# Performance work log

Hardware: AMD Instinct MI355X
Metric: run time of the kernel (lower is better)

Reference implementation:

```python
import jax, jax.numpy as jnp
import numpy as np

N_EMBD = 128
N_HEADS = 8
HEAD_SIZE = N_EMBD // N_HEADS  # 16
EPS = 1e-5


def _layernorm(x, g, b):
    m = jnp.mean(x, axis=-1, keepdims=True)
    v = jnp.mean(jnp.square(x - m), axis=-1, keepdims=True)
    return (x - m) * jax.lax.rsqrt(v + EPS) * g + b


def setup_inputs() -> dict:
    key = jax.random.key(0)
    ks = jax.random.split(key, 12)
    B, T, D, H, HS = 16, 1024, N_EMBD, N_HEADS, HEAD_SIZE
    s = 1.0 / np.sqrt(D)
    inp = {
        "x": jax.random.normal(ks[0], (B, T, D), jnp.float32),
        # per-head QKV projections (stacked over heads; matches ModuleList of Linear(D, HS))
        "Wq": jax.random.uniform(ks[1], (H, D, HS), jnp.float32, -s, s),
        "bq": jnp.zeros((H, HS), jnp.float32),
        "Wk": jax.random.uniform(ks[2], (H, D, HS), jnp.float32, -s, s),
        "bk": jnp.zeros((H, HS), jnp.float32),
        "Wv": jax.random.uniform(ks[3], (H, D, HS), jnp.float32, -s, s),
        "bv": jnp.zeros((H, HS), jnp.float32),
        "Wp": jax.random.uniform(ks[4], (H * HS, D), jnp.float32, -s, s),
        "bp": jnp.zeros((D,), jnp.float32),
        "W1": jax.random.uniform(ks[5], (D, 4 * D), jnp.float32, -s, s),
        "b1": jnp.zeros((4 * D,), jnp.float32),
        "W2": jax.random.uniform(ks[6], (4 * D, D), jnp.float32, -1.0 / np.sqrt(4 * D), 1.0 / np.sqrt(4 * D)),
        "b2": jnp.zeros((D,), jnp.float32),
        "g1": jnp.ones((D,), jnp.float32),
        "be1": jnp.zeros((D,), jnp.float32),
        "g2": jnp.ones((D,), jnp.float32),
        "be2": jnp.zeros((D,), jnp.float32),
    }
    return inp


def reference(x, Wq, bq, Wk, bk, Wv, bv, Wp, bp, W1, b1, W2, b2, g1, be1, g2, be2):
    B, T, D = x.shape
    # batched per-head projections: [B,T,D] x [H,D,HS] -> [B,H,T,HS]
    q = jnp.einsum("btd,hds->bhts", x, Wq) + bq[None, :, None, :]
    k = jnp.einsum("btd,hds->bhts", x, Wk) + bk[None, :, None, :]
    v = jnp.einsum("btd,hds->bhts", x, Wv) + bv[None, :, None, :]
    scores = jnp.einsum("bhts,bhus->bhtu", q, k) / np.sqrt(HEAD_SIZE).astype(np.float32)
    tril = jnp.tril(jnp.ones((T, T), x.dtype))
    # faithful to source: multiplicative + additive mask (not -inf where)
    scores = scores * tril - 1e12 * (1.0 - tril)
    attn = jax.nn.softmax(scores, axis=-1)
    out = jnp.einsum("bhtu,bhus->bhts", attn, v)  # [B,H,T,HS]
    # concat heads in head order -> [B,T,H*HS]
    out = out.transpose(0, 2, 1, 3).reshape(B, T, -1)
    attn_out = out @ Wp + bp
    x = _layernorm(attn_out + x, g1, be1)
    h = jax.nn.gelu(x @ W1 + b1, approximate=False) @ W2 + b2
    x = _layernorm(h + x, g2, be2)
    return x
```

## Files before the change

kernel.cpp:

```cpp
#include <hip/hip_runtime.h>
#include <hip/hip_bf16.h>
#include <math.h>

constexpr int NB  = 16;
constexpr int NT  = 1024;
constexpr int ND  = 128;
constexpr int NH  = 8;
constexpr int NHS = 16;
constexpr int NDH = 512;
constexpr long NBT = (long)NB * NT;

typedef __attribute__((ext_vector_type(8))) short short8;
typedef __attribute__((ext_vector_type(4))) float f32x4;
typedef __attribute__((ext_vector_type(4))) unsigned short us4;

__device__ __forceinline__ unsigned short f2bf(float f) {
    __hip_bfloat16 h = __float2bfloat16(f);
    return *(unsigned short*)&h;
}

__device__ __forceinline__ short8 cvt8(const float* p) {
    const float4 f0 = *(const float4*)p;
    const float4 f1 = *(const float4*)(p + 4);
    union { short8 s; __hip_bfloat162 h[4]; } u;
    u.h[0] = __float22bfloat162_rn(make_float2(f0.x, f0.y));
    u.h[1] = __float22bfloat162_rn(make_float2(f0.z, f0.w));
    u.h[2] = __float22bfloat162_rn(make_float2(f1.x, f1.y));
    u.h[3] = __float22bfloat162_rn(make_float2(f1.z, f1.w));
    return u.s;
}

__device__ __forceinline__ float fast_gelu(float y) {
    const float t = y * y;
    const float u = __builtin_fmaf(y * 0.044715f, t, y);
    const float e = __builtin_amdgcn_exp2f(u * -2.302118131f);
    return y * __builtin_amdgcn_rcpf(1.0f + e);
}

__global__ __launch_bounds__(256) void k_prep(
    const float* __restrict__ Wq, const float* __restrict__ Wk,
    const float* __restrict__ Wv, __hip_bfloat16* __restrict__ Wqkvt)
{
    const int blk = blockIdx.x, tid = threadIdx.x;
    const int i0 = blk * 1024 + tid * 4;
    const int n = i0 >> 7, d0 = i0 & 127;
    const int sec = n >> 7, m = n & 127;
    const float* W = (sec == 0) ? Wq : (sec == 1) ? Wk : Wv;
    const float* src = W + (m >> 4) * 2048 + (m & 15);
    us4 v;
    #pragma unroll
    for (int j = 0; j < 4; ++j) v[j] = f2bf(src[(d0 + j) * 16]);
    *(us4*)((unsigned short*)Wqkvt + i0) = v;
}

__global__ __launch_bounds__(256) void k_qkv(
    const float* __restrict__ x, const __hip_bfloat16* __restrict__ Wqkvt,
    const float* __restrict__ bq, const float* __restrict__ bk,
    const float* __restrict__ bv,
    const float* __restrict__ Wp, const float* __restrict__ W1,
    const float* __restrict__ W2,
    __hip_bfloat16* __restrict__ Wpt, __hip_bfloat16* __restrict__ W1t,
    __hip_bfloat16* __restrict__ W2t,
    __hip_bfloat16* __restrict__ qo, __hip_bfloat16* __restrict__ ko,
    __hip_bfloat16* __restrict__ vo)
{
    __shared__ __align__(16) unsigned short st[32 * 392];
    const int tid = threadIdx.x;

    if (blockIdx.x >= 512) {
        const int blk = blockIdx.x - 512 + 48;
        us4 v;
        if (blk < 64) {
            const int i0 = (blk - 48) * 1024 + tid * 4;
            const int n = i0 >> 7, d0 = i0 & 127;
            #pragma unroll
            for (int j = 0; j < 4; ++j) v[j] = f2bf(Wp[(d0 + j) * 128 + n]);
            *(us4*)((unsigned short*)Wpt + i0) = v;
        } else if (blk < 128) {
            const int i0 = (blk - 64) * 1024 + tid * 4;
            const int n = i0 >> 7, d0 = i0 & 127;
            #pragma unroll
            for (int j = 0; j < 4; ++j) v[j] = f2bf(W1[(d0 + j) * 512 + n]);
            *(us4*)((unsigned short*)W1t + i0) = v;
        } else {
            const int i0 = (blk - 128) * 1024 + tid * 4;
            const int n = i0 >> 9, k0 = i0 & 511;
            #pragma unroll
            for (int j = 0; j < 4; ++j) v[j] = f2bf(W2[(k0 + j) * 128 + n]);
            *(us4*)((unsigned short*)W2t + i0) = v;
        }
        return;
    }

    const int w    = tid >> 6;
    const int lane = tid & 63;
    const int sL   = lane & 15;
    const int quad = lane >> 4;
    const int tok0 = blockIdx.x * 32;

    const unsigned short* W = (const unsigned short*)Wqkvt;

    short8 bx[2][4];
    #pragma unroll
    for (int tt = 0; tt < 2; ++tt)
        #pragma unroll
        for (int ks = 0; ks < 4; ++ks)
            bx[tt][ks] = cvt8(x + (size_t)(tok0 + tt * 16 + sL) * 128 + ks * 32 + quad * 8);

    f32x4 acc[6][2];
    #pragma unroll
    for (int ci = 0; ci < 6; ++ci)
        #pragma unroll
        for (int tt = 0; tt < 2; ++tt)
            acc[ci][tt] = (f32x4){0.f, 0.f, 0.f, 0.f};

    #pragma unroll
    for (int ks = 0; ks < 4; ++ks) {
        short8 aW[6];
        #pragma unroll
        for (int ci = 0; ci < 6; ++ci) {
            const int ct = w * 6 + ci;
            aW[ci] = *(const short8*)(W + (size_t)(ct * 16 + sL) * 128 + ks * 32 + quad * 8);
        }
        #pragma unroll
        for (int ci = 0; ci < 6; ++ci)
            #pragma unroll
            for (int tt = 0; tt < 2; ++tt)
                acc[ci][tt] = __builtin_amdgcn_mfma_f32_16x16x32_bf16(aW[ci], bx[tt][ks], acc[ci][tt], 0, 0, 0);
    }

    const float qscale = 0.3606737602f;
    #pragma unroll
    for (int ci = 0; ci < 6; ++ci) {
        const int ct = w * 6 + ci;
        const int kind = ct >> 3;
        const int ncc = (ct & 7) * 16 + quad * 4;
        const float4 bb = *(const float4*)(((kind == 0) ? bq : (kind == 1) ? bk : bv) + ncc);
        #pragma unroll
        for (int tt = 0; tt < 2; ++tt) {
            us4 v;
            #pragma unroll
            for (int r = 0; r < 4; ++r) {
                float val = acc[ci][tt][r] + ((const float*)&bb)[r];
                if (kind == 0) val *= qscale;
                v[r] = f2bf(val);
            }
            *(us4*)(st + (tt * 16 + sL) * 392 + ct * 16 + quad * 4) = v;
        }
    }
    __syncthreads();

    const int b = tok0 >> 10, tt0 = tok0 & 1023;
    {
        const int h = tid >> 5, tok = tid & 31;
        const unsigned short* sq = st + tok * 392 + h * 16;
        const unsigned short* sk = st + tok * 392 + 128 + h * 16;
        unsigned short* dq = (unsigned short*)qo + ((size_t)(b * 8 + h) * 1024 + tt0 + tok) * 16;
        unsigned short* dk = (unsigned short*)ko + ((size_t)(b * 8 + h) * 1024 + tt0 + tok) * 16;
        *(short8*)dq       = *(const short8*)sq;
        *(short8*)(dq + 8) = *(const short8*)(sq + 8);
        *(short8*)dk       = *(const short8*)sk;
        *(short8*)(dk + 8) = *(const short8*)(sk + 8);
    }
    if (tid < 128) {
        const int h = tid >> 4, s = tid & 15;
        unsigned short tmp[32];
        #pragma unroll
        for (int tok = 0; tok < 32; ++tok)
            tmp[tok] = st[tok * 392 + 256 + h * 16 + s];
        unsigned short* dv = (unsigned short*)vo + ((size_t)(b * 8 + h) * 16 + s) * 1024 + tt0;
        #pragma unroll
        for (int j = 0; j < 4; ++j)
            *(short8*)(dv + j * 8) = *(const short8*)(tmp + j * 8);
    }
}

__global__ __launch_bounds__(256) void k_attn(
    const __hip_bfloat16* __restrict__ qb, const __hip_bfloat16* __restrict__ kb,
    const __hip_bfloat16* __restrict__ vtb, __hip_bfloat16* __restrict__ att)
{
    const int bh   = blockIdx.x & 127;
    const int sub  = blockIdx.x >> 7;
    const int wave = threadIdx.x >> 6;
    const int lane = threadIdx.x & 63;
    const int sL   = lane & 15;
    const int q    = lane >> 4;
    const int b = bh >> 3, h = bh & 7;
    const int tile = sub * 4 + wave;

    const char* qbase = (const char*)qb  + (size_t)bh * NT * NHS * 2;
    const char* kbase = (const char*)kb  + (size_t)bh * NT * NHS * 2;
    const char* vbase = (const char*)vtb + (size_t)bh * NHS * NT * 2;

    const short8 zz = {0,0,0,0,0,0,0,0};

    const int t0 = tile * 16;
    const int tmy = t0 + sL;

    short8 bQ = zz;
    if (q < 2) bQ = *(const short8*)(qbase + (size_t)tmy * 32 + q * 16);

    f32x4 o = {0.f, 0.f, 0.f, 0.f};
    float lp = 0.f;

    const int nch = (t0 + 47) >> 5;
    for (int c = 0; c < nch; ++c) {
        const int u0 = c * 32;
        short8 aK0 = zz, aK1 = zz;
        if (q < 2) {
            aK0 = *(const short8*)(kbase + (size_t)(u0 + sL) * 32 + q * 16);
            aK1 = *(const short8*)(kbase + (size_t)(u0 + 16 + sL) * 32 + q * 16);
        }
        const f32x4 zc = {0.f, 0.f, 0.f, 0.f};
        f32x4 sT0 = __builtin_amdgcn_mfma_f32_16x16x32_bf16(aK0, bQ, zc, 0, 0, 0);
        f32x4 sT1 = __builtin_amdgcn_mfma_f32_16x16x32_bf16(aK1, bQ, zc, 0, 0, 0);

        int pk[4];
        if (u0 + 31 <= t0) {
            #pragma unroll
            for (int r = 0; r < 4; ++r) {
                const float p0 = __builtin_amdgcn_exp2f(sT0[r]);
                const float p1 = __builtin_amdgcn_exp2f(sT1[r]);
                lp += p0 + p1;
                __hip_bfloat162 hh = __float22bfloat162_rn(make_float2(p0, p1));
                pk[r] = *(int*)&hh;
            }
        } else {
            #pragma unroll
            for (int r = 0; r < 4; ++r) {
                const int ua = u0 + 4 * q + r;
                const float e0 = __builtin_amdgcn_exp2f(sT0[r]);
                const float e1 = __builtin_amdgcn_exp2f(sT1[r]);
                const float p0 = (ua      <= tmy) ? e0 : 0.f;
                const float p1 = (ua + 16 <= tmy) ? e1 : 0.f;
                lp += p0 + p1;
                __hip_bfloat162 hh = __float22bfloat162_rn(make_float2(p0, p1));
                pk[r] = *(int*)&hh;
            }
        }

        short8 bP;
        #pragma unroll
        for (int j = 0; j < 8; ++j) {
            const int srcq = ((q & 1) << 1) + (j >> 2);
            const int src  = (srcq << 4) + sL;
            const int g = __shfl(pk[j & 3], src);
            bP[j] = (short)((q < 2) ? (g & 0xffff) : ((unsigned)g >> 16));
        }

        const short8 aV = *(const short8*)(vbase + ((size_t)sL * NT + u0 + q * 8) * 2);
        o = __builtin_amdgcn_mfma_f32_16x16x32_bf16(aV, bP, o, 0, 0, 0);
    }

    float l = lp;
    l += __shfl_xor(l, 16);
    l += __shfl_xor(l, 32);
    const float inv = 1.0f / l;
    us4 res;
    res[0] = f2bf(o[0] * inv); res[1] = f2bf(o[1] * inv);
    res[2] = f2bf(o[2] * inv); res[3] = f2bf(o[3] * inv);
    *(us4*)((unsigned short*)att + ((size_t)b * NT + tmy) * ND + h * NHS + q * 4) = res;
}

__global__ __launch_bounds__(256) void k_tail(
    const __hip_bfloat16* __restrict__ attb, const __hip_bfloat16* __restrict__ Wpt,
    const __hip_bfloat16* __restrict__ W1t, const __hip_bfloat16* __restrict__ W2t,
    const float* __restrict__ x, const float* __restrict__ bp,
    const float* __restrict__ g1, const float* __restrict__ be1,
    const float* __restrict__ b1, const float* __restrict__ b2,
    const float* __restrict__ g2, const float* __restrict__ be2,
    float* __restrict__ out)
{
    __shared__ float ys[32][132];
    __shared__ __align__(16) unsigned short l1b[32 * 136];
    __shared__ __align__(16) unsigned short midb[32 * 528];
    const int w    = threadIdx.x >> 6;
    const int lane = threadIdx.x & 63;
    const int sL   = lane & 15;
    const int quad = lane >> 4;
    const int tok0 = blockIdx.x * 32;

    {
        const unsigned short* A = (const unsigned short*)attb;
        const unsigned short* W = (const unsigned short*)Wpt;
        short8 bfr[2][4];
        #pragma unroll
        for (int tt = 0; tt < 2; ++tt)
            #pragma unroll
            for (int ks = 0; ks < 4; ++ks)
                bfr[tt][ks] = *(const short8*)(A + (size_t)(tok0 + tt * 16 + sL) * 128 + ks * 32 + quad * 8);

        f32x4 acc[2][2];
        #pragma unroll
        for (int ci = 0; ci < 2; ++ci)
            #pragma unroll
            for (int tt = 0; tt < 2; ++tt)
                acc[ci][tt] = (f32x4){0.f, 0.f, 0.f, 0.f};

        #pragma unroll
        for (int ks = 0; ks < 4; ++ks) {
            short8 aW[2];
            #pragma unroll
            for (int ci = 0; ci < 2; ++ci)
                aW[ci] = *(const short8*)(W + (size_t)((w * 2 + ci) * 16 + sL) * 128 + ks * 32 + quad * 8);
            #pragma unroll
            for (int ci = 0; ci < 2; ++ci)
                #pragma unroll
                for (int tt = 0; tt < 2; ++tt)
                    acc[ci][tt] = __builtin_amdgcn_mfma_f32_16x16x32_bf16(aW[ci], bfr[tt][ks], acc[ci][tt], 0, 0, 0);
        }
        #pragma unroll
        for (int ci = 0; ci < 2; ++ci) {
            const int n0 = (w * 2 + ci) * 16 + quad * 4;
            const float4 bb = *(const float4*)(bp + n0);
            #pragma unroll
            for (int tt = 0; tt < 2; ++tt) {
                float4 v;
                v.x = acc[ci][tt][0] + bb.x; v.y = acc[ci][tt][1] + bb.y;
                v.z = acc[ci][tt][2] + bb.z; v.w = acc[ci][tt][3] + bb.w;
                *(float4*)(&ys[tt * 16 + sL][n0]) = v;
            }
        }
    }
    __syncthreads();

    const int tok = threadIdx.x >> 3;
    const int l8  = threadIdx.x & 7;
    const int c0  = l8 * 16;
    {
        float vals[16];
        float s = 0.f, s2 = 0.f;
        #pragma unroll
        for (int ch = 0; ch < 4; ++ch) {
            const float4 ly = *(const float4*)&ys[tok][c0 + ch * 4];
            const float4 gx = *(const float4*)(x + (size_t)(tok0 + tok) * 128 + c0 + ch * 4);
            vals[ch*4+0] = ly.x + gx.x; vals[ch*4+1] = ly.y + gx.y;
            vals[ch*4+2] = ly.z + gx.z; vals[ch*4+3] = ly.w + gx.w;
            #pragma unroll
            for (int j = 0; j < 4; ++j) { s += vals[ch*4+j]; s2 += vals[ch*4+j] * vals[ch*4+j]; }
        }
        #pragma unroll
        for (int off = 1; off <= 4; off <<= 1) {
            s  += __shfl_xor(s, off, 8);
            s2 += __shfl_xor(s2, off, 8);
        }
        const float mean = s * (1.0f / 128.0f);
        const float var  = s2 * (1.0f / 128.0f) - mean * mean;
        const float rstd = rsqrtf(var + 1e-5f);
        #pragma unroll
        for (int ch = 0; ch < 4; ++ch) {
            const float4 gg = *(const float4*)(g1 + c0 + ch * 4);
            const float4 bb = *(const float4*)(be1 + c0 + ch * 4);
            float ln0 = (vals[ch*4+0] - mean) * rstd * gg.x + bb.x;
            float ln1v = (vals[ch*4+1] - mean) * rstd * gg.y + bb.y;
            float ln2v = (vals[ch*4+2] - mean) * rstd * gg.z + bb.z;
            float ln3 = (vals[ch*4+3] - mean) * rstd * gg.w + bb.w;
            ys[tok][c0 + ch*4 + 0] = ln0;
            ys[tok][c0 + ch*4 + 1] = ln1v;
            ys[tok][c0 + ch*4 + 2] = ln2v;
            ys[tok][c0 + ch*4 + 3] = ln3;
            us4 lb;
            lb[0] = f2bf(ln0); lb[1] = f2bf(ln1v); lb[2] = f2bf(ln2v); lb[3] = f2bf(ln3);
            *(us4*)(l1b + tok * 136 + c0 + ch * 4) = lb;
        }
    }
    __syncthreads();

    {
        const unsigned short* W = (const unsigned short*)W1t;
        short8 bl[2][4];
        #pragma unroll
        for (int tt = 0; tt < 2; ++tt)
            #pragma unroll
            for (int ks = 0; ks < 4; ++ks)
                bl[tt][ks] = *(const short8*)(l1b + (tt * 16 + sL) * 136 + ks * 32 + quad * 8);

        f32x4 acc[8][2];
        #pragma unroll
        for (int ci = 0; ci < 8; ++ci)
            #pragma unroll
            for (int tt = 0; tt < 2; ++tt)
                acc[ci][tt] = (f32x4){0.f, 0.f, 0.f, 0.f};

        #pragma unroll
        for (int ks = 0; ks < 4; ++ks) {
            short8 aW[8];
            #pragma unroll
            for (int ci = 0; ci < 8; ++ci)
                aW[ci] = *(const short8*)(W + (size_t)((w * 8 + ci) * 16 + sL) * 128 + ks * 32 + quad * 8);
            #pragma unroll
            for (int ci = 0; ci < 8; ++ci)
                #pragma unroll
                for (int tt = 0; tt < 2; ++tt)
                    acc[ci][tt] = __builtin_amdgcn_mfma_f32_16x16x32_bf16(aW[ci], bl[tt][ks], acc[ci][tt], 0, 0, 0);
        }
        #pragma unroll
        for (int ci = 0; ci < 8; ++ci) {
            const int n0 = (w * 8 + ci) * 16 + quad * 4;
            const float4 bb = *(const float4*)(b1 + n0);
            #pragma unroll
            for (int tt = 0; tt < 2; ++tt) {
                us4 v;
                v[0] = f2bf(fast_gelu(acc[ci][tt][0] + bb.x));
                v[1] = f2bf(fast_gelu(acc[ci][tt][1] + bb.y));
                v[2] = f2bf(fast_gelu(acc[ci][tt][2] + bb.z));
                v[3] = f2bf(fast_gelu(acc[ci][tt][3] + bb.w));
                *(us4*)(midb + (tt * 16 + sL) * 528 + n0) = v;
            }
        }
    }
    __syncthreads();

    f32x4 acc2[2][2];
    #pragma unroll
    for (int ci = 0; ci < 2; ++ci)
        #pragma unroll
        for (int tt = 0; tt < 2; ++tt)
            acc2[ci][tt] = (f32x4){0.f, 0.f, 0.f, 0.f};
    {
        const unsigned short* W = (const unsigned short*)W2t;
        #pragma unroll
        for (int ks = 0; ks < 16; ++ks) {
            short8 bm0 = *(const short8*)(midb + (size_t)sL * 528 + ks * 32 + quad * 8);
            short8 bm1 = *(const short8*)(midb + (size_t)(16 + sL) * 528 + ks * 32 + quad * 8);
            short8 aW0 = *(const short8*)(W + (size_t)((w * 2) * 16 + sL) * 512 + ks * 32 + quad * 8);
            short8 aW1 = *(const short8*)(W + (size_t)((w * 2 + 1) * 16 + sL) * 512 + ks * 32 + quad * 8);
            acc2[0][0] = __builtin_amdgcn_mfma_f32_16x16x32_bf16(aW0, bm0, acc2[0][0], 0, 0, 0);
            acc2[0][1] = __builtin_amdgcn_mfma_f32_16x16x32_bf16(aW0, bm1, acc2[0][1], 0, 0, 0);
            acc2[1][0] = __builtin_amdgcn_mfma_f32_16x16x32_bf16(aW1, bm0, acc2[1][0], 0, 0, 0);
            acc2[1][1] = __builtin_amdgcn_mfma_f32_16x16x32_bf16(aW1, bm1, acc2[1][1], 0, 0, 0);
        }
    }
    __syncthreads();
    float* ys2 = (float*)midb;
    #pragma unroll
    for (int ci = 0; ci < 2; ++ci) {
        const int n0 = (w * 2 + ci) * 16 + quad * 4;
        const float4 bb = *(const float4*)(b2 + n0);
        #pragma unroll
        for (int tt = 0; tt < 2; ++tt) {
            float4 v;
            v.x = acc2[ci][tt][0] + bb.x; v.y = acc2[ci][tt][1] + bb.y;
            v.z = acc2[ci][tt][2] + bb.z; v.w = acc2[ci][tt][3] + bb.w;
            *(float4*)(ys2 + (tt * 16 + sL) * 132 + n0) = v;
        }
    }
    __syncthreads();

    {
        float vals[16];
        float s = 0.f, s2 = 0.f;
        #pragma unroll
        for (int ch = 0; ch < 4; ++ch) {
            const float4 ly = *(const float4*)(ys2 + tok * 132 + c0 + ch * 4);
            const float4 gx = *(const float4*)&ys[tok][c0 + ch * 4];
            vals[ch*4+0] = ly.x + gx.x; vals[ch*4+1] = ly.y + gx.y;
            vals[ch*4+2] = ly.z + gx.z; vals[ch*4+3] = ly.w + gx.w;
            #pragma unroll
            for (int j = 0; j < 4; ++j) { s += vals[ch*4+j]; s2 += vals[ch*4+j] * vals[ch*4+j]; }
        }
        #pragma unroll
        for (int off = 1; off <= 4; off <<= 1) {
            s  += __shfl_xor(s, off, 8);
            s2 += __shfl_xor(s2, off, 8);
        }
        const float mean = s * (1.0f / 128.0f);
        const float var  = s2 * (1.0f / 128.0f) - mean * mean;
        const float rstd = rsqrtf(var + 1e-5f);
        #pragma unroll
        for (int ch = 0; ch < 4; ++ch) {
            const float4 gg = *(const float4*)(g2 + c0 + ch * 4);
            const float4 bb = *(const float4*)(be2 + c0 + ch * 4);
            float4 ln;
            ln.x = (vals[ch*4+0] - mean) * rstd * gg.x + bb.x;
            ln.y = (vals[ch*4+1] - mean) * rstd * gg.y + bb.y;
            ln.z = (vals[ch*4+2] - mean) * rstd * gg.z + bb.z;
            ln.w = (vals[ch*4+3] - mean) * rstd * gg.w + bb.w;
            *(float4*)(out + (size_t)(tok0 + tok) * 128 + c0 + ch * 4) = ln;
        }
    }
}

extern "C" void kernel_launch(void* const* d_in, const int* in_sizes, int n_in,
                              void* d_out, int out_size, void* d_ws, size_t ws_size,
                              hipStream_t stream)
{
    (void)in_sizes; (void)n_in; (void)out_size; (void)ws_size;
    const float* x   = (const float*)d_in[0];
    const float* Wq  = (const float*)d_in[1];
    const float* bq  = (const float*)d_in[2];
    const float* Wk  = (const float*)d_in[3];
    const float* bk  = (const float*)d_in[4];
    const float* Wv  = (const float*)d_in[5];
    const float* bv  = (const float*)d_in[6];
    const float* Wp  = (const float*)d_in[7];
    const float* bp  = (const float*)d_in[8];
    const float* W1  = (const float*)d_in[9];
    const float* b1  = (const float*)d_in[10];
    const float* W2  = (const float*)d_in[11];
    const float* b2  = (const float*)d_in[12];
    const float* g1  = (const float*)d_in[13];
    const float* be1 = (const float*)d_in[14];
    const float* g2  = (const float*)d_in[15];
    const float* be2 = (const float*)d_in[16];
    float* out = (float*)d_out;

    char* wsb = (char*)d_ws;
    __hip_bfloat16* qb   = (__hip_bfloat16*)wsb;
    __hip_bfloat16* kb   = (__hip_bfloat16*)(wsb + (4u  << 20));
    __hip_bfloat16* vtb  = (__hip_bfloat16*)(wsb + (8u  << 20));
    __hip_bfloat16* attb = (__hip_bfloat16*)(wsb + (12u << 20));
    __hip_bfloat16* Wqkvt= (__hip_bfloat16*)(wsb + (16u << 20));
    __hip_bfloat16* Wpt  = (__hip_bfloat16*)(wsb + (16u << 20) + (96u  << 10));
    __hip_bfloat16* W1t  = (__hip_bfloat16*)(wsb + (16u << 20) + (128u << 10));
    __hip_bfloat16* W2t  = (__hip_bfloat16*)(wsb + (16u << 20) + (256u << 10));

    k_prep<<<48,   256, 0, stream>>>(Wq, Wk, Wv, Wqkvt);
    k_qkv <<<656,  256, 0, stream>>>(x, Wqkvt, bq, bk, bv, Wp, W1, W2,
                                     Wpt, W1t, W2t, qb, kb, vtb);
    k_attn<<<2048, 256, 0, stream>>>(qb, kb, vtb, attb);
    k_tail<<<512,  256, 0, stream>>>(attb, Wpt, W1t, W2t, x, bp, g1, be1,
                                     b1, b2, g2, be2, out);
}
```

Baseline: 162.5 us.

## Rewrite causal attention with 32x32x16 MFMA tiles and permlane32 swaps

```diff
diff --git a/kernel.cpp b/kernel.cpp
--- a/kernel.cpp
+++ b/kernel.cpp
@@ -12,6 +12,7 @@
 
 typedef __attribute__((ext_vector_type(8))) short short8;
 typedef __attribute__((ext_vector_type(4))) float f32x4;
+typedef __attribute__((ext_vector_type(16))) float f32x16;
 typedef __attribute__((ext_vector_type(4))) unsigned short us4;
 
 __device__ __forceinline__ unsigned short f2bf(float f) {
@@ -179,87 +180,101 @@
     const __hip_bfloat16* __restrict__ qb, const __hip_bfloat16* __restrict__ kb,
     const __hip_bfloat16* __restrict__ vtb, __hip_bfloat16* __restrict__ att)
 {
+    __shared__ __align__(16) float stg[4][32 * 16];
     const int bh   = blockIdx.x & 127;
     const int sub  = blockIdx.x >> 7;
     const int wave = threadIdx.x >> 6;
     const int lane = threadIdx.x & 63;
-    const int sL   = lane & 15;
-    const int q    = lane >> 4;
+    const int col  = lane & 31;
+    const int hi   = lane >> 5;
     const int b = bh >> 3, h = bh & 7;
     const int tile = sub * 4 + wave;
-
-    const char* qbase = (const char*)qb  + (size_t)bh * NT * NHS * 2;
-    const char* kbase = (const char*)kb  + (size_t)bh * NT * NHS * 2;
-    const char* vbase = (const char*)vtb + (size_t)bh * NHS * NT * 2;
-
-    const short8 zz = {0,0,0,0,0,0,0,0};
-
-    const int t0 = tile * 16;
-    const int tmy = t0 + sL;
-
-    short8 bQ = zz;
-    if (q < 2) bQ = *(const short8*)(qbase + (size_t)tmy * 32 + q * 16);
-
-    f32x4 o = {0.f, 0.f, 0.f, 0.f};
-    float lp = 0.f;
-
-    const int nch = (t0 + 47) >> 5;
-    for (int c = 0; c < nch; ++c) {
+    const int t0 = tile * 32;
+
+    const unsigned short* qp = (const unsigned short*)qb  + (size_t)bh * NT * NHS;
+    const unsigned short* kp = (const unsigned short*)kb  + (size_t)bh * NT * NHS;
+    const unsigned short* vp = (const unsigned short*)vtb + (size_t)bh * NHS * NT;
+
+    const short8 bQ = *(const short8*)(qp + (size_t)(t0 + col) * NHS + hi * 8);
+    const unsigned short* vrow = vp + (size_t)(col & 15) * NT + hi * 8;
+
+    f32x16 o;
+    #pragma unroll
+    for (int r = 0; r < 16; ++r) o[r] = 0.f;
+    f32x16 zc;
+    #pragma unroll
+    for (int r = 0; r < 16; ++r) zc[r] = 0.f;
+    float lp0 = 0.f, lp1 = 0.f, lp2 = 0.f, lp3 = 0.f;
+
+    for (int c = 0; c <= tile; ++c) {
         const int u0 = c * 32;
-        short8 aK0 = zz, aK1 = zz;
-        if (q < 2) {
-            aK0 = *(const short8*)(kbase + (size_t)(u0 + sL) * 32 + q * 16);
-            aK1 = *(const short8*)(kbase + (size_t)(u0 + 16 + sL) * 32 + q * 16);
-        }
-        const f32x4 zc = {0.f, 0.f, 0.f, 0.f};
-        f32x4 sT0 = __builtin_amdgcn_mfma_f32_16x16x32_bf16(aK0, bQ, zc, 0, 0, 0);
-        f32x4 sT1 = __builtin_amdgcn_mfma_f32_16x16x32_bf16(aK1, bQ, zc, 0, 0, 0);
-
-        int pk[4];
-        if (u0 + 31 <= t0) {
-            #pragma unroll
-            for (int r = 0; r < 4; ++r) {
-                const float p0 = __builtin_amdgcn_exp2f(sT0[r]);
-                const float p1 = __builtin_amdgcn_exp2f(sT1[r]);
-                lp += p0 + p1;
-                __hip_bfloat162 hh = __float22bfloat162_rn(make_float2(p0, p1));
-                pk[r] = *(int*)&hh;
+        const short8 aK  = *(const short8*)(kp + (size_t)(u0 + col) * NHS + hi * 8);
+        const short8 bV0 = *(const short8*)(vrow + u0);
+        const short8 bV1 = *(const short8*)(vrow + u0 + 16);
+
+        const f32x16 sT = __builtin_amdgcn_mfma_f32_32x32x16_bf16(aK, bQ, zc, 0, 0, 0);
+
+        float p[16];
+        if (c < tile) {
+            #pragma unroll
+            for (int r = 0; r < 16; ++r) p[r] = __builtin_amdgcn_exp2f(sT[r]);
+        } else {
+            const int kh = 4 * hi;
+            #pragma unroll
+            for (int r = 0; r < 16; ++r) {
+                const int kc = (r & 3) + 8 * (r >> 2) + kh;
+                const float e = __builtin_amdgcn_exp2f(sT[r]);
+                p[r] = (kc <= col) ? e : 0.f;
             }
-        } else {
-            #pragma unroll
-            for (int r = 0; r < 4; ++r) {
-                const int ua = u0 + 4 * q + r;
-                const float e0 = __builtin_amdgcn_exp2f(sT0[r]);
-                const float e1 = __builtin_amdgcn_exp2f(sT1[r]);
-                const float p0 = (ua      <= tmy) ? e0 : 0.f;
-                const float p1 = (ua + 16 <= tmy) ? e1 : 0.f;
-                lp += p0 + p1;
-                __hip_bfloat162 hh = __float22bfloat162_rn(make_float2(p0, p1));
-                pk[r] = *(int*)&hh;
-            }
-        }
-
-        short8 bP;
-        #pragma unroll
-        for (int j = 0; j < 8; ++j) {
-            const int srcq = ((q & 1) << 1) + (j >> 2);
-            const int src  = (srcq << 4) + sL;
-            const int g = __shfl(pk[j & 3], src);
-            bP[j] = (short)((q < 2) ? (g & 0xffff) : ((unsigned)g >> 16));
-        }
-
-        const short8 aV = *(const short8*)(vbase + ((size_t)sL * NT + u0 + q * 8) * 2);
-        o = __builtin_amdgcn_mfma_f32_16x16x32_bf16(aV, bP, o, 0, 0, 0);
-    }
-
-    float l = lp;
-    l += __shfl_xor(l, 16);
-    l += __shfl_xor(l, 32);
-    const float inv = 1.0f / l;
-    us4 res;
-    res[0] = f2bf(o[0] * inv); res[1] = f2bf(o[1] * inv);
-    res[2] = f2bf(o[2] * inv); res[3] = f2bf(o[3] * inv);
-    *(us4*)((unsigned short*)att + ((size_t)b * NT + tmy) * ND + h * NHS + q * 4) = res;
+        }
+        #pragma unroll
+        for (int r = 0; r < 16; r += 4) {
+            lp0 += p[r]; lp1 += p[r + 1]; lp2 += p[r + 2]; lp3 += p[r + 3];
+        }
+
+        int d[8];
+        #pragma unroll
+        for (int i = 0; i < 8; ++i) {
+            __hip_bfloat162 hh = __float22bfloat162_rn(make_float2(p[2 * i], p[2 * i + 1]));
+            d[i] = *(int*)&hh;
+        }
+        auto s0 = __builtin_amdgcn_permlane32_swap(d[0], d[2], false, false);
+        auto s1 = __builtin_amdgcn_permlane32_swap(d[1], d[3], false, false);
+        auto s2 = __builtin_amdgcn_permlane32_swap(d[4], d[6], false, false);
+        auto s3 = __builtin_amdgcn_permlane32_swap(d[5], d[7], false, false);
+        union { int i[4]; short8 v; } A0, A1;
+        A0.i[0] = s0[0]; A0.i[1] = s1[0]; A0.i[2] = s0[1]; A0.i[3] = s1[1];
+        A1.i[0] = s2[0]; A1.i[1] = s3[0]; A1.i[2] = s2[1]; A1.i[3] = s3[1];
+
+        o = __builtin_amdgcn_mfma_f32_32x32x16_bf16(A0.v, bV0, o, 0, 0, 0);
+        o = __builtin_amdgcn_mfma_f32_32x32x16_bf16(A1.v, bV1, o, 0, 0, 0);
+    }
+
+    float lp = (lp0 + lp1) + (lp2 + lp3);
+    lp += __shfl_xor(lp, 32);
+    const float inv = 1.0f / lp;
+
+    float* sp = stg[wave];
+    if (col < 16) {
+        #pragma unroll
+        for (int r = 0; r < 16; ++r) {
+            const int qr = (r & 3) + 8 * (r >> 2) + 4 * hi;
+            sp[qr * 16 + col] = o[r];
+        }
+    }
+    __syncthreads();
+    const float invq = __shfl(inv, lane >> 1);
+    const float* rp = sp + (lane >> 1) * 16 + (lane & 1) * 8;
+    const float4 va = *(const float4*)rp;
+    const float4 vb = *(const float4*)(rp + 4);
+    union { short8 v; unsigned short u[8]; } res;
+    res.u[0] = f2bf(va.x * invq); res.u[1] = f2bf(va.y * invq);
+    res.u[2] = f2bf(va.z * invq); res.u[3] = f2bf(va.w * invq);
+    res.u[4] = f2bf(vb.x * invq); res.u[5] = f2bf(vb.y * invq);
+    res.u[6] = f2bf(vb.z * invq); res.u[7] = f2bf(vb.w * invq);
+    unsigned short* dst = (unsigned short*)att +
+        ((size_t)b * NT + t0 + (lane >> 1)) * ND + h * NHS + (lane & 1) * 8;
+    *(short8*)dst = res.v;
 }
 
 __global__ __launch_bounds__(256) void k_tail(
@@ -518,7 +533,7 @@
     k_prep<<<48,   256, 0, stream>>>(Wq, Wk, Wv, Wqkvt);
     k_qkv <<<656,  256, 0, stream>>>(x, Wqkvt, bq, bk, bv, Wp, W1, W2,
                                      Wpt, W1t, W2t, qb, kb, vtb);
-    k_attn<<<2048, 256, 0, stream>>>(qb, kb, vtb, attb);
+    k_attn<<<1024, 256, 0, stream>>>(qb, kb, vtb, attb);
     k_tail<<<512,  256, 0, stream>>>(attb, Wpt, W1t, W2t, x, bp, g1, be1,
                                      b1, b2, g2, be2, out);
 }
```

Result: no change. 160.0 us (-1.5%).
